# Kernel tuning notes

Hardware: AMD Instinct MI355X
Metric: run time of the kernel (lower is better)

Reference implementation:

```python
import jax, jax.numpy as jnp
import numpy as np

# Dimensions (match init_kwargs / input_specs)
B, T, H, S, R, E = 4, 2048, 1024, 512, 16, 4
F = 6 + 2 * R           # engine_state_feature_dim
ETA = 0.1               # impression_rate
ACC_DECAY = 0.99        # accumulator EMA decay
EPS = 1e-6


def setup_inputs() -> dict:
    key = jax.random.key(0)
    ks = jax.random.split(key, 20)
    n = jax.random.normal
    x = n(ks[0], (B, T, H), jnp.float32)
    # ComplexLinear signal_proj: hidden -> state
    sig_Wr = n(ks[1], (H, S), jnp.float32) / np.sqrt(H).astype(np.float32)
    sig_Wi = n(ks[2], (H, S), jnp.float32) / np.sqrt(H).astype(np.float32)
    sig_br = jnp.zeros((S,), jnp.float32)
    sig_bi = jnp.zeros((S,), jnp.float32)
    # Per-engine complex state projection [E, S, R] and diagonal complex decay [E, R]
    A_r = n(ks[3], (E, S, R), jnp.float32) / np.sqrt(S).astype(np.float32)
    A_i = n(ks[4], (E, S, R), jnp.float32) / np.sqrt(S).astype(np.float32)
    mag = 0.90 + 0.09 * jax.random.uniform(ks[5], (E, R), jnp.float32)
    ph = (2.0 * np.pi) * jax.random.uniform(ks[6], (E, R), jnp.float32)
    lam_r = mag * jnp.cos(ph)
    lam_i = mag * jnp.sin(ph)
    # Per-engine ComplexLinear: feature(F) -> hidden(H)
    eh_Wr = n(ks[7], (E, F, H), jnp.float32) / np.sqrt(F).astype(np.float32)
    eh_Wi = n(ks[8], (E, F, H), jnp.float32) / np.sqrt(F).astype(np.float32)
    eh_br = jnp.zeros((E, H), jnp.float32)
    eh_bi = jnp.zeros((E, H), jnp.float32)
    # Engine fusion ComplexLinear: E*H -> H
    fu_Wr = n(ks[9], (E * H, H), jnp.float32) / np.sqrt(E * H).astype(np.float32)
    fu_Wi = n(ks[10], (E * H, H), jnp.float32) / np.sqrt(E * H).astype(np.float32)
    fu_br = jnp.zeros((H,), jnp.float32)
    fu_bi = jnp.zeros((H,), jnp.float32)
    # Gate: Linear(4H -> H)
    g_W = n(ks[11], (4 * H, H), jnp.float32) / np.sqrt(4 * H).astype(np.float32)
    g_b = jnp.zeros((H,), jnp.float32)
    return dict(x=x, sig_Wr=sig_Wr, sig_Wi=sig_Wi, sig_br=sig_br, sig_bi=sig_bi,
                A_r=A_r, A_i=A_i, lam_r=lam_r, lam_i=lam_i,
                eh_Wr=eh_Wr, eh_Wi=eh_Wi, eh_br=eh_br, eh_bi=eh_bi,
                fu_Wr=fu_Wr, fu_Wi=fu_Wi, fu_br=fu_br, fu_bi=fu_bi,
                g_W=g_W, g_b=g_b)


def _run_engines(ur, ui, lam_r, lam_i):
    """Complex diagonal recurrence over time for all engines jointly.
    ur, ui: [E,B,T,R] complex drive. Returns per-step features [E,B,T,F] (real, imag)."""
    lr = lam_r[:, None, :]  # [E,1,R]
    li = lam_i[:, None, :]

    def step(carry, u):
        hr, hi, acc = carry                      # [E,B,R], [E,B,R], [E,B]
        ur_t, ui_t = u                           # [E,B,R]
        nhr = (1.0 - ETA) * (lr * hr - li * hi) + ETA * ur_t
        nhi = (1.0 - ETA) * (lr * hi + li * hr) + ETA * ui_t
        mag2 = nhr * nhr + nhi * nhi             # [E,B,R]
        m_mean = jnp.mean(mag2, axis=-1)         # [E,B]
        nacc = ACC_DECAY * acc + (1.0 - ACC_DECAY) * m_mean
        inv = jax.lax.rsqrt(m_mean + EPS)[..., None]
        hnr, hni = nhr * inv, nhi * inv          # rms-normalized complex state
        z = jnp.zeros_like(m_mean)
        scal_r = jnp.stack([hnr.mean(-1), hni.mean(-1),
                            jnp.sqrt(m_mean + EPS),
                            jnp.sqrt(jnp.max(mag2, axis=-1) + EPS),
                            nacc, jnp.log1p(nacc)], axis=-1)   # [E,B,6]
        scal_i = jnp.stack([hni.mean(-1), -hnr.mean(-1), z, z, z, z], axis=-1)
        fr = jnp.concatenate([scal_r, hnr, hni], axis=-1)      # [E,B,F]
        fi = jnp.concatenate([scal_i, hni, -hnr], axis=-1)
        return (nhr, nhi, nacc), (fr, fi)

    init = (jnp.zeros((E, B, R), ur.dtype), jnp.zeros((E, B, R), ur.dtype),
            jnp.zeros((E, B), ur.dtype))
    u_seq = (jnp.moveaxis(ur, 2, 0), jnp.moveaxis(ui, 2, 0))   # [T,E,B,R]
    _, (frs, fis) = jax.lax.scan(step, init, u_seq)
    return jnp.moveaxis(frs, 0, 2), jnp.moveaxis(fis, 0, 2)    # [E,B,T,F]


def reference(x, sig_Wr, sig_Wi, sig_br, sig_bi, A_r, A_i, lam_r, lam_i,
              eh_Wr, eh_Wi, eh_br, eh_bi, fu_Wr, fu_Wi, fu_br, fu_bi, g_W, g_b):
    # Complex signal projection of real input: z = (Wr + i Wi)^T x + b
    zr = x @ sig_Wr + sig_br                     # [B,T,S]
    zi = x @ sig_Wi + sig_bi
    # Complex per-engine drive u = A^H-style complex matmul: [E,B,T,R]
    ur = jnp.einsum('bts,esr->ebtr', zr, A_r) - jnp.einsum('bts,esr->ebtr', zi, A_i)
    ui = jnp.einsum('bts,esr->ebtr', zr, A_i) + jnp.einsum('bts,esr->ebtr', zi, A_r)
    fr, fi = _run_engines(ur, ui, lam_r, lam_i)  # [E,B,T,F]
    # Per-engine ComplexLinear feature -> hidden
    yr = (jnp.einsum('ebtf,efh->ebth', fr, eh_Wr)
          - jnp.einsum('ebtf,efh->ebth', fi, eh_Wi)) + eh_br[:, None, None, :]
    yi = (jnp.einsum('ebtf,efh->ebth', fr, eh_Wi)
          + jnp.einsum('ebtf,efh->ebth', fi, eh_Wr)) + eh_bi[:, None, None, :]
    # Concat engines along feature axis -> [B,T,E*H]
    yr_c = jnp.moveaxis(yr, 0, 2).reshape(B, T, E * H)
    yi_c = jnp.moveaxis(yi, 0, 2).reshape(B, T, E * H)
    # Engine fusion ComplexLinear
    frf = yr_c @ fu_Wr - yi_c @ fu_Wi + fu_br    # [B,T,H]
    fif = yr_c @ fu_Wi + yi_c @ fu_Wr + fu_bi
    mag = jnp.sqrt(frf * frf + fif * fif + EPS)
    g = jax.nn.sigmoid(jnp.concatenate([x, frf, fif, mag], axis=-1) @ g_W + g_b)
    return g * frf + (1.0 - g) * x
```

## Files before the change

### kernel.cpp

```cpp
#include <hip/hip_runtime.h>
#include <stdint.h>

#define B_ 4
#define T_ 2048
#define H_ 1024
#define S_ 512
#define R_ 16
#define E_ 4
#define F_ 38
#define BT_ (B_*T_)
#define KF_ 320

typedef __attribute__((ext_vector_type(8))) __bf16 bf16x8;
typedef __attribute__((ext_vector_type(4))) float f32x4;

static __device__ __forceinline__ unsigned short f2bf(float f) {
    unsigned int u = __float_as_uint(f);
    unsigned int r = (u + 0x7fffu + ((u >> 16) & 1u)) >> 16;
    return (unsigned short)r;
}

static __device__ __forceinline__ void gload_lds16(const unsigned short* g, unsigned short* l) {
    __builtin_amdgcn_global_load_lds(
        (const __attribute__((address_space(1))) unsigned int*)g,
        (__attribute__((address_space(3))) unsigned int*)l, 16, 0, 0);
}

template<int EPI>
__global__ __launch_bounds__(256) void k_gemm(
    const unsigned short* __restrict__ A, int lda,
    const unsigned short* __restrict__ BT, int ldb,
    float* __restrict__ C, int ldc,
    const float* __restrict__ bias, int K,
    size_t sA, size_t sB, size_t sC, int nbx,
    const float* __restrict__ aux1, const float* __restrict__ aux2,
    unsigned short* __restrict__ auxO)
{
    A  += (size_t)blockIdx.z * sA;
    BT += (size_t)blockIdx.z * sB;
    C  += (size_t)blockIdx.z * sC;

    int bx, by;
    {
        const int f = blockIdx.x;
        const int nwg = gridDim.x;
        int s;
        if ((nwg & 7) == 0) {
            const int q = nwg >> 3;
            s = (f & 7) * q + (f >> 3);
        } else s = f;
        by = s / nbx; bx = s - by * nbx;
    }

    __shared__ unsigned short As[2 * 4096];
    __shared__ unsigned short Bs[2 * 4096];
    const int tid = threadIdx.x;
    const int l = tid & 63;
    const int wv = tid >> 6;
    const int wm = wv >> 1, wn = wv & 1;
    const int m16 = l & 15, kg = l >> 4;
    const size_t bm = (size_t)by * 128;
    const size_t bn = (size_t)bx * 128;

    const int slab0 = wv * 2, slab1 = wv * 2 + 1;
    const int rIn = l >> 2;
    const int kOff = (l & 3) * 8;
    const unsigned short* gA0 = A + (bm + slab0 * 16 + rIn) * (size_t)lda + kOff;
    const unsigned short* gA1 = A + (bm + slab1 * 16 + rIn) * (size_t)lda + kOff;
    const unsigned short* gB0 = BT + (bn + slab0 * 16 + rIn) * (size_t)ldb + kOff;
    const unsigned short* gB1 = BT + (bn + slab1 * 16 + rIn) * (size_t)ldb + kOff;
    const int sOffA0 = slab0 * 512, sOffA1 = slab1 * 512;

    f32x4 acc[4][4];
#pragma unroll
    for (int i = 0; i < 4; ++i)
#pragma unroll
        for (int j = 0; j < 4; ++j) acc[i][j] = (f32x4){0.f, 0.f, 0.f, 0.f};

    const int nkt = K >> 5;
    gload_lds16(gA0, As + sOffA0);
    gload_lds16(gA1, As + sOffA1);
    gload_lds16(gB0, Bs + sOffA0);
    gload_lds16(gB1, Bs + sOffA1);
    gA0 += 32; gA1 += 32; gB0 += 32; gB1 += 32;
    __syncthreads();

    for (int kt = 0; kt < nkt; ++kt) {
        const int cur = (kt & 1) * 4096;
        const int nxt = 4096 - cur;
        if (kt + 1 < nkt) {
            gload_lds16(gA0, As + nxt + sOffA0);
            gload_lds16(gA1, As + nxt + sOffA1);
            gload_lds16(gB0, Bs + nxt + sOffA0);
            gload_lds16(gB1, Bs + nxt + sOffA1);
            gA0 += 32; gA1 += 32; gB0 += 32; gB1 += 32;
        }
        bf16x8 af[4], bfr[4];
#pragma unroll
        for (int i = 0; i < 4; ++i)
            af[i] = *(const bf16x8*)&As[cur + (wm * 64 + i * 16 + m16) * 32 + kg * 8];
#pragma unroll
        for (int j = 0; j < 4; ++j)
            bfr[j] = *(const bf16x8*)&Bs[cur + (wn * 64 + j * 16 + m16) * 32 + kg * 8];
#pragma unroll
        for (int i = 0; i < 4; ++i)
#pragma unroll
            for (int j = 0; j < 4; ++j)
                acc[i][j] = __builtin_amdgcn_mfma_f32_16x16x32_bf16(af[i], bfr[j], acc[i][j], 0, 0, 0);
        __syncthreads();
    }

#pragma unroll
    for (int j = 0; j < 4; ++j) {
        const size_t col = bn + wn * 64 + j * 16 + m16;
        const float bv = (EPI == 1) ? 0.f : (bias ? bias[col] : 0.f);
#pragma unroll
        for (int i = 0; i < 4; ++i) {
            const size_t row0 = bm + wm * 64 + i * 16 + kg * 4;
#pragma unroll
            for (int p = 0; p < 4; ++p) {
                const size_t row = row0 + p;
                if constexpr (EPI == 0) {
                    C[row * (size_t)ldc + col] = acc[i][j][p] + bv;
                } else if constexpr (EPI == 1) {
                    atomicAdd(&C[row * (size_t)ldc + col], acc[i][j][p]);
                } else if constexpr (EPI == 2) {
                    const float v = acc[i][j][p] + bv;
                    const float w = __shfl_xor(v, 1, 64);
                    const int h = (int)(col >> 1);
                    if ((col & 1) == 0) {
                        C[row * 1024 + h] = v;
                        auxO[row * 4096 + 1024 + h] = f2bf(v);
                    } else {
                        auxO[row * 4096 + 2048 + h] = f2bf(v);
                        auxO[row * 4096 + 3072 + h] = f2bf(sqrtf(w * w + v * v + 1e-6f));
                    }
                } else {
                    const float z = acc[i][j][p] + bv;
                    const float g = 1.f / (1.f + __expf(-z));
                    const float fr = aux1[row * 1024 + col];
                    const float xv = aux2[row * 1024 + col];
                    C[row * 1024 + col] = fmaf(g, fr - xv, xv);
                }
            }
        }
    }
}

__global__ __launch_bounds__(256) void k_cast_x(const float* __restrict__ x,
                                                unsigned short* __restrict__ Abig)
{
    const int gid = blockIdx.x * 256 + threadIdx.x;
    const int row = gid >> 8;
    const int c4 = (gid & 255) << 2;
    float4 v = *(const float4*)&x[(size_t)row * H_ + c4];
    ushort4 o;
    o.x = f2bf(v.x); o.y = f2bf(v.y); o.z = f2bf(v.z); o.w = f2bf(v.w);
    *(ushort4*)&Abig[(size_t)row * 4096 + c4] = o;
}

__global__ __launch_bounds__(256) void k_gwt(const float* __restrict__ gW,
                                             unsigned short* __restrict__ gWT)
{
    __shared__ float tile[32][33];
    const int tx = threadIdx.x & 31, ty = threadIdx.x >> 5;
    const int k0 = blockIdx.x * 32, n0 = blockIdx.y * 32;
#pragma unroll
    for (int q = 0; q < 4; ++q) {
        int kk = ty * 4 + q;
        tile[kk][tx] = gW[(size_t)(k0 + kk) * H_ + n0 + tx];
    }
    __syncthreads();
#pragma unroll
    for (int q = 0; q < 4; ++q) {
        int nn = ty * 4 + q;
        gWT[(size_t)(n0 + nn) * 4096 + k0 + tx] = f2bf(tile[tx][nn]);
    }
}

__global__ __launch_bounds__(64) void k_wu(const float* __restrict__ sigWr,
                                           const float* __restrict__ sigWi,
                                           const float* __restrict__ A_r,
                                           const float* __restrict__ A_i,
                                           unsigned short* __restrict__ WuT)
{
    __shared__ float swr[S_], swi[S_];
    const int h = blockIdx.x;
    const int tid = threadIdx.x;
    for (int s = tid; s < S_; s += 64) {
        swr[s] = sigWr[(size_t)h * S_ + s];
        swi[s] = sigWi[(size_t)h * S_ + s];
    }
    __syncthreads();
    const int e = tid >> 4, r = tid & 15;
    float a0 = 0.f, a1 = 0.f;
    for (int s = 0; s < S_; ++s) {
        float ar = A_r[((size_t)(e * S_ + s)) * R_ + r];
        float ai = A_i[((size_t)(e * S_ + s)) * R_ + r];
        float wr = swr[s], wi = swi[s];
        a0 += wr * ar - wi * ai;
        a1 += wr * ai + wi * ar;
    }
    WuT[(size_t)tid * H_ + h] = f2bf(a0);
    WuT[(size_t)(64 + tid) * H_ + h] = f2bf(a1);
}

__global__ __launch_bounds__(64) void k_bu(const float* __restrict__ sigbr,
                                           const float* __restrict__ sigbi,
                                           const float* __restrict__ A_r,
                                           const float* __restrict__ A_i,
                                           float* __restrict__ b_u)
{
    const int n = blockIdx.x;
    const int lane = threadIdx.x;
    const int m = n & 63;
    const int e = m >> 4, r = m & 15;
    const bool hi = n >= 64;
    float acc = 0.f;
    for (int s = lane; s < S_; s += 64) {
        float ar = A_r[((size_t)(e * S_ + s)) * R_ + r];
        float ai = A_i[((size_t)(e * S_ + s)) * R_ + r];
        float br = sigbr[s], bi = sigbi[s];
        acc += hi ? (br * ai + bi * ar) : (br * ar - bi * ai);
    }
#pragma unroll
    for (int st = 32; st; st >>= 1) acc += __shfl_down(acc, st, 64);
    if (lane == 0) b_u[n] = acc;
}

__global__ __launch_bounds__(256) void k_uinit(const float* __restrict__ b_u,
                                               float* __restrict__ U)
{
    const int gid = blockIdx.x * 256 + threadIdx.x;
    U[gid] = b_u[gid & 127];
}

__global__ __launch_bounds__(256) void k_prepA(const float* __restrict__ ehWr,
                                               const float* __restrict__ ehWi,
                                               const float* __restrict__ ehbr,
                                               const float* __restrict__ ehbi,
                                               unsigned short* __restrict__ Ac)
{
    const int gid = blockIdx.x * 256 + threadIdx.x;
    const int e = gid >> 16;
    const int rem = gid & 65535;
    const int row = rem >> 9;
    const int k = (rem & 511) << 2;
    float4 f = {0.f, 0.f, 0.f, 0.f};
    if (row < F_) {
        const float* src = (k < 1024) ? ehWr + ((size_t)(e * F_ + row)) * 1024 + k
                                      : ehWi + ((size_t)(e * F_ + row)) * 1024 + (k - 1024);
        f = *(const float4*)src;
    } else if (row == F_) {
        const float* src = (k < 1024) ? ehbr + (size_t)e * 1024 + k
                                      : ehbi + (size_t)e * 1024 + (k - 1024);
        f = *(const float4*)src;
    }
    ushort4 o;
    o.x = f2bf(f.x); o.y = f2bf(f.y); o.z = f2bf(f.z); o.w = f2bf(f.w);
    *(ushort4*)&Ac[(size_t)gid * 4] = o;
}

__global__ __launch_bounds__(256) void k_prepB(const float* __restrict__ fuWr,
                                               const float* __restrict__ fuWi,
                                               unsigned short* __restrict__ Bc)
{
    __shared__ float tR[32][33], tI[32][33];
    const int e = blockIdx.z;
    const int k0 = blockIdx.x * 32;
    const int h0 = blockIdx.y * 32;
    const int tx = threadIdx.x & 31, ty = threadIdx.x >> 5;
    const float* fr = fuWr + ((size_t)e * 1024 + k0) * 1024 + h0;
    const float* fi = fuWi + ((size_t)e * 1024 + k0) * 1024 + h0;
#pragma unroll
    for (int q = 0; q < 4; ++q) {
        int kk = ty * 4 + q;
        tR[kk][tx] = fr[(size_t)kk * 1024 + tx];
        tI[kk][tx] = fi[(size_t)kk * 1024 + tx];
    }
    __syncthreads();
    unsigned short* Be = Bc + (size_t)e * 2048 * 2048;
#pragma unroll
    for (int q = 0; q < 4; ++q) {
        int rr = ty * 4 + q;
        float vR = tR[tx][rr], vI = tI[tx][rr];
        size_t rowLo = (size_t)(h0 + rr) * 2048;
        size_t rowHi = (size_t)(1024 + h0 + rr) * 2048;
        Be[rowLo + k0 + tx]        = f2bf(vR);
        Be[rowLo + 1024 + k0 + tx] = f2bf(-vI);
        Be[rowHi + k0 + tx]        = f2bf(vI);
        Be[rowHi + 1024 + k0 + tx] = f2bf(vR);
    }
}

__global__ __launch_bounds__(256) void k_w2t(const float* __restrict__ C,
                                             unsigned short* __restrict__ W2T)
{
    const int gid = blockIdx.x * 256 + threadIdx.x;
    const int n = gid / KF_;
    const int k = gid - n * KF_;
    const int h = n >> 1;
    const int s = n & 1;
    float v = 0.f;
    if (k < 304) {
        const int fp = (k < 152) ? k : k - 152;
        const int e = fp / F_;
        const int f = fp - e * F_;
        const float* Ce = C + ((size_t)e * 128 + f) * 2048;
        const float mr = Ce[h], mi = Ce[1024 + h];
        if (s == 0) v = (k < 152) ? mr : -mi;
        else        v = (k < 152) ? mi :  mr;
    }
    W2T[gid] = f2bf(v);
}

__global__ __launch_bounds__(256) void k_b2(const float* __restrict__ fubr,
                                            const float* __restrict__ fubi,
                                            const float* __restrict__ C,
                                            float* __restrict__ b2)
{
    const int n = blockIdx.x * 256 + threadIdx.x;
    const int h = n >> 1;
    const int s = n & 1;
    const int colOld = s * 1024 + h;
    float v = s ? fubi[h] : fubr[h];
#pragma unroll
    for (int e = 0; e < 4; ++e)
        v += C[(size_t)e * 128 * 2048 + (size_t)F_ * 2048 + colOld];
    b2[n] = v;
}

__global__ __launch_bounds__(64) void k_scan(const float* __restrict__ U,
                                             const float* __restrict__ lam_r,
                                             const float* __restrict__ lam_i,
                                             float* __restrict__ Hr, float* __restrict__ Hi)
{
    const int wid = blockIdx.x;
    const int b = wid >> 6, ch = wid & 63;
    const int lane = threadIdx.x;
    const float cr = 0.9f * lam_r[ch];
    const float ci = 0.9f * lam_i[ch];
    const float* Ub = U + (size_t)b * T_ * 128;
    const int t0 = lane * 32;
    float ur[32], ui[32];
#pragma unroll
    for (int j = 0; j < 32; ++j) {
        ur[j] = Ub[(size_t)(t0 + j) * 128 + ch];
        ui[j] = Ub[(size_t)(t0 + j) * 128 + 64 + ch];
    }
    float hr = 0.f, hi = 0.f;
#pragma unroll
    for (int j = 0; j < 32; ++j) {
        float nr = fmaf(cr, hr, fmaf(-ci, hi, 0.1f * ur[j]));
        float ni = fmaf(cr, hi, fmaf(ci, hr, 0.1f * ui[j]));
        hr = nr; hi = ni;
    }
    float dr = cr, di = ci;
#pragma unroll
    for (int q = 0; q < 5; ++q) { float t = dr*dr - di*di; di = 2.f*dr*di; dr = t; }
    float xr = hr, xi = hi;
#pragma unroll
    for (int st = 1; st < 64; st <<= 1) {
        float yr = __shfl_up(xr, (unsigned)st, 64);
        float yi = __shfl_up(xi, (unsigned)st, 64);
        if (lane >= st) {
            float nxr = fmaf(dr, yr, fmaf(-di, yi, xr));
            float nxi = fmaf(dr, yi, fmaf(di, yr, xi));
            xr = nxr; xi = nxi;
        }
        float t = dr*dr - di*di; di = 2.f*dr*di; dr = t;
    }
    float ir = __shfl_up(xr, 1u, 64);
    float ii = __shfl_up(xi, 1u, 64);
    if (lane == 0) { ir = 0.f; ii = 0.f; }
    hr = ir; hi = ii;
    float* HrB = Hr + (size_t)b * T_ * 64;
    float* HiB = Hi + (size_t)b * T_ * 64;
#pragma unroll
    for (int j = 0; j < 32; ++j) {
        float nr = fmaf(cr, hr, fmaf(-ci, hi, 0.1f * ur[j]));
        float ni = fmaf(cr, hi, fmaf(ci, hr, 0.1f * ui[j]));
        HrB[(size_t)(t0 + j) * 64 + ch] = nr;
        HiB[(size_t)(t0 + j) * 64 + ch] = ni;
        hr = nr; hi = ni;
    }
}

__global__ __launch_bounds__(256) void k_feat(const float* __restrict__ Hr,
                                              const float* __restrict__ Hi,
                                              unsigned short* __restrict__ Fcat,
                                              float* __restrict__ Mbuf)
{
    const int gid = blockIdx.x * 256 + threadIdx.x;
    const int e = gid & 3;
    const int bt = gid >> 2;
    const float* hr = Hr + (size_t)bt * 64 + e * 16;
    const float* hi = Hi + (size_t)bt * 64 + e * 16;
    float nr[16], ni[16];
#pragma unroll
    for (int q = 0; q < 4; ++q) {
        float4 vr = ((const float4*)hr)[q];
        float4 vi = ((const float4*)hi)[q];
        nr[q*4+0]=vr.x; nr[q*4+1]=vr.y; nr[q*4+2]=vr.z; nr[q*4+3]=vr.w;
        ni[q*4+0]=vi.x; ni[q*4+1]=vi.y; ni[q*4+2]=vi.z; ni[q*4+3]=vi.w;
    }
    float sum = 0.f, mx = 0.f, sr = 0.f, si = 0.f;
#pragma unroll
    for (int i = 0; i < 16; ++i) {
        float m2 = nr[i] * nr[i] + ni[i] * ni[i];
        sum += m2; mx = fmaxf(mx, m2);
        sr += nr[i]; si += ni[i];
    }
    const float mm = sum * 0.0625f;
    const float inv = rsqrtf(mm + 1e-6f);
    const int b = bt >> 11, t = bt & (T_ - 1);
    Mbuf[(size_t)(e * 4 + b) * T_ + t] = mm;
    unsigned short* Fp = Fcat + (size_t)bt * KF_;
    const int br = e * F_, bi2 = 152 + e * F_;
    const float mhr = sr * 0.0625f * inv;
    const float mhi = si * 0.0625f * inv;
    Fp[br + 0] = f2bf(mhr);
    Fp[br + 1] = f2bf(mhi);
    Fp[br + 2] = f2bf(sqrtf(mm + 1e-6f));
    Fp[br + 3] = f2bf(sqrtf(mx + 1e-6f));
    Fp[bi2 + 0] = f2bf(mhi);
    Fp[bi2 + 1] = f2bf(-mhr);
#pragma unroll
    for (int i = 0; i < 16; ++i) {
        float a = nr[i] * inv, c = ni[i] * inv;
        Fp[br + 6 + i]   = f2bf(a);
        Fp[br + 22 + i]  = f2bf(c);
        Fp[bi2 + 6 + i]  = f2bf(c);
        Fp[bi2 + 22 + i] = f2bf(-a);
    }
}

__global__ __launch_bounds__(256) void k_acc(const float* __restrict__ Mbuf,
                                             unsigned short* __restrict__ Fcat)
{
    const int w = blockIdx.x * 4 + (threadIdx.x >> 6);
    const int lane = threadIdx.x & 63;
    const int e = w >> 2, b = w & 3;
    const float* mp = Mbuf + (size_t)(e * 4 + b) * T_ + lane * 32;
    float m[32];
#pragma unroll
    for (int j = 0; j < 32; ++j) m[j] = mp[j];
    float s = 0.f;
#pragma unroll
    for (int j = 0; j < 32; ++j) s = fmaf(0.99f, s, 0.01f * m[j]);
    float d = 0.99f;
#pragma unroll
    for (int q = 0; q < 5; ++q) d = d * d;
    float x = s;
#pragma unroll
    for (int st = 1; st < 64; st <<= 1) {
        float y = __shfl_up(x, (unsigned)st, 64);
        if (lane >= st) x = fmaf(d, y, x);
        d = d * d;
    }
    float init = __shfl_up(x, 1u, 64);
    if (lane == 0) init = 0.f;
    float acc = init;
#pragma unroll
    for (int j = 0; j < 32; ++j) {
        acc = fmaf(0.99f, acc, 0.01f * m[j]);
        const int t = lane * 32 + j;
        size_t ro = ((size_t)(b * T_ + t)) * KF_ + e * F_;
        Fcat[ro + 4] = f2bf(acc);
        Fcat[ro + 5] = f2bf(log1pf(acc));
    }
}

extern "C" void kernel_launch(void* const* d_in, const int* in_sizes, int n_in,
                              void* d_out, int out_size, void* d_ws, size_t ws_size,
                              hipStream_t stream)
{
    const float* x     = (const float*)d_in[0];
    const float* sigWr = (const float*)d_in[1];
    const float* sigWi = (const float*)d_in[2];
    const float* sigbr = (const float*)d_in[3];
    const float* sigbi = (const float*)d_in[4];
    const float* A_r   = (const float*)d_in[5];
    const float* A_i   = (const float*)d_in[6];
    const float* lam_r = (const float*)d_in[7];
    const float* lam_i = (const float*)d_in[8];
    const float* ehWr  = (const float*)d_in[9];
    const float* ehWi  = (const float*)d_in[10];
    const float* ehbr  = (const float*)d_in[11];
    const float* ehbi  = (const float*)d_in[12];
    const float* fuWr  = (const float*)d_in[13];
    const float* fuWi  = (const float*)d_in[14];
    const float* fubr  = (const float*)d_in[15];
    const float* fubi  = (const float*)d_in[16];
    const float* gW    = (const float*)d_in[17];
    const float* gb    = (const float*)d_in[18];

    char* ws = (char*)d_ws;
    size_t off = 0;
    auto alloc = [&](size_t bytes) -> void* {
        void* p = ws + off;
        off = (off + bytes + 255) & ~(size_t)255;
        return p;
    };
    unsigned short* Abig = (unsigned short*)alloc((size_t)BT_ * 4096 * 2);
    float* FRFr          = (float*)alloc((size_t)BT_ * 1024 * 4);
    unsigned short* Fcat = (unsigned short*)alloc((size_t)BT_ * KF_ * 2);
    float* U             = (float*)alloc((size_t)BT_ * 128 * 4);
    float* Hr            = (float*)alloc((size_t)BT_ * 64 * 4);
    float* Hi            = (float*)alloc((size_t)BT_ * 64 * 4);
    float* Mbuf          = (float*)alloc((size_t)16 * T_ * 4);
    unsigned short* WuT  = (unsigned short*)alloc((size_t)128 * H_ * 2);
    float* b_u           = (float*)alloc(128 * 4);
    unsigned short* W2T  = (unsigned short*)alloc((size_t)2048 * KF_ * 2);
    float* b2            = (float*)alloc(2048 * 4);
    unsigned short* gWT  = (unsigned short*)alloc((size_t)H_ * 4096 * 2);
    unsigned short* Acomp= (unsigned short*)alloc((size_t)4 * 128 * 2048 * 2);
    unsigned short* Bcomp= (unsigned short*)alloc((size_t)4 * 2048 * 2048 * 2);
    float* Ccomp         = (float*)alloc((size_t)4 * 128 * 2048 * 4);
    if (off > ws_size) return;

    hipMemsetAsync(Fcat, 0, (size_t)BT_ * KF_ * 2, stream);

    k_cast_x<<<dim3(BT_ * H_ / 4 / 256), dim3(256), 0, stream>>>(x, Abig);
    k_gwt<<<dim3(128, 32), dim3(256), 0, stream>>>(gW, gWT);
    k_wu<<<dim3(H_), dim3(64), 0, stream>>>(sigWr, sigWi, A_r, A_i, WuT);
    k_bu<<<dim3(128), dim3(64), 0, stream>>>(sigbr, sigbi, A_r, A_i, b_u);
    k_prepA<<<dim3(1024), dim3(256), 0, stream>>>(ehWr, ehWi, ehbr, ehbi, Acomp);
    k_prepB<<<dim3(32, 32, 4), dim3(256), 0, stream>>>(fuWr, fuWi, Bcomp);

    k_gemm<0><<<dim3(16, 1, 4), dim3(256), 0, stream>>>(
        Acomp, 2048, Bcomp, 2048, Ccomp, 2048, (const float*)nullptr, 2048,
        (size_t)128 * 2048, (size_t)2048 * 2048, (size_t)128 * 2048, 16,
        nullptr, nullptr, nullptr);

    k_w2t<<<dim3(2048 * KF_ / 256), dim3(256), 0, stream>>>(Ccomp, W2T);
    k_b2<<<dim3(8), dim3(256), 0, stream>>>(fubr, fubi, Ccomp, b2);

    k_uinit<<<dim3(BT_ * 128 / 256), dim3(256), 0, stream>>>(b_u, U);
    k_gemm<1><<<dim3(64, 1, 4), dim3(256), 0, stream>>>(
        Abig, 4096, WuT, H_, U, 128, (const float*)nullptr, 256,
        (size_t)256, (size_t)256, (size_t)0, 1, nullptr, nullptr, nullptr);

    k_scan<<<dim3(B_ * 64), dim3(64), 0, stream>>>(U, lam_r, lam_i, Hr, Hi);
    k_feat<<<dim3(BT_ * E_ / 256), dim3(256), 0, stream>>>(Hr, Hi, Fcat, Mbuf);
    k_acc<<<dim3(4), dim3(256), 0, stream>>>(Mbuf, Fcat);

    k_gemm<2><<<dim3(1024, 1, 1), dim3(256), 0, stream>>>(
        Fcat, KF_, W2T, KF_, FRFr, 1024, b2, KF_,
        (size_t)0, (size_t)0, (size_t)0, 16, nullptr, nullptr, Abig);

    k_gemm<3><<<dim3(512, 1, 1), dim3(256), 0, stream>>>(
        Abig, 4096, gWT, 4096, (float*)d_out, 1024, gb, 4096,
        (size_t)0, (size_t)0, (size_t)0, 8, FRFr, x, nullptr);
}
```

Baseline: 392.0 us.

## Deepen GEMM LDS pipeline, split-K the fusion precompute, transpose U layout

The GEMM kernel gains a templated pipeline depth. Up to four LDS stages are kept in flight, with explicit vmcnt waits and raw barriers replacing the per-iteration __syncthreads. The weight-composition GEMM is split along K into four chunks accumulated with atomics into a zeroed buffer, which raises its block count from 64 to 256. The U projection now writes a transposed layout so the scan can read time-contiguous float4 vectors instead of strided scalars. These changes add LDS usage, which can lower occupancy, plus atomic traffic and an extra memset.

```diff
diff --git a/kernel.cpp b/kernel.cpp
--- a/kernel.cpp
+++ b/kernel.cpp
@@ -26,19 +26,20 @@
         (__attribute__((address_space(3))) unsigned int*)l, 16, 0, 0);
 }
 
-template<int EPI>
+template<int EPI, int DEPTH>
 __global__ __launch_bounds__(256) void k_gemm(
     const unsigned short* __restrict__ A, int lda,
     const unsigned short* __restrict__ BT, int ldb,
     float* __restrict__ C, int ldc,
     const float* __restrict__ bias, int K,
-    size_t sA, size_t sB, size_t sC, int nbx,
+    size_t sA, size_t sB, size_t sC, size_t sA2, size_t sB2, int nbx,
     const float* __restrict__ aux1, const float* __restrict__ aux2,
     unsigned short* __restrict__ auxO)
 {
-    A  += (size_t)blockIdx.z * sA;
-    BT += (size_t)blockIdx.z * sB;
-    C  += (size_t)blockIdx.z * sC;
+    const int z1 = blockIdx.z >> 2, z0 = blockIdx.z & 3;
+    A  += (size_t)z1 * sA + (size_t)z0 * sA2;
+    BT += (size_t)z1 * sB + (size_t)z0 * sB2;
+    C  += (size_t)z1 * sC;
 
     int bx, by;
     {
@@ -52,8 +53,8 @@
         by = s / nbx; bx = s - by * nbx;
     }
 
-    __shared__ unsigned short As[2 * 4096];
-    __shared__ unsigned short Bs[2 * 4096];
+    __shared__ unsigned short As[DEPTH * 4096];
+    __shared__ unsigned short Bs[DEPTH * 4096];
     const int tid = threadIdx.x;
     const int l = tid & 63;
     const int wv = tid >> 6;
@@ -78,23 +79,37 @@
         for (int j = 0; j < 4; ++j) acc[i][j] = (f32x4){0.f, 0.f, 0.f, 0.f};
 
     const int nkt = K >> 5;
-    gload_lds16(gA0, As + sOffA0);
-    gload_lds16(gA1, As + sOffA1);
-    gload_lds16(gB0, Bs + sOffA0);
-    gload_lds16(gB1, Bs + sOffA1);
-    gA0 += 32; gA1 += 32; gB0 += 32; gB1 += 32;
-    __syncthreads();
-
-    for (int kt = 0; kt < nkt; ++kt) {
-        const int cur = (kt & 1) * 4096;
-        const int nxt = 4096 - cur;
-        if (kt + 1 < nkt) {
-            gload_lds16(gA0, As + nxt + sOffA0);
-            gload_lds16(gA1, As + nxt + sOffA1);
-            gload_lds16(gB0, Bs + nxt + sOffA0);
-            gload_lds16(gB1, Bs + nxt + sOffA1);
+#pragma unroll
+    for (int p = 0; p < DEPTH - 1; ++p) {
+        if (p < nkt) {
+            const int o = p * 4096;
+            gload_lds16(gA0, As + o + sOffA0);
+            gload_lds16(gA1, As + o + sOffA1);
+            gload_lds16(gB0, Bs + o + sOffA0);
+            gload_lds16(gB1, Bs + o + sOffA1);
             gA0 += 32; gA1 += 32; gB0 += 32; gB1 += 32;
         }
+    }
+
+    for (int kt = 0; kt < nkt; ++kt) {
+        __builtin_amdgcn_s_barrier();
+        if (kt + DEPTH - 1 < nkt) {
+            const int o = ((kt + DEPTH - 1) % DEPTH) * 4096;
+            gload_lds16(gA0, As + o + sOffA0);
+            gload_lds16(gA1, As + o + sOffA1);
+            gload_lds16(gB0, Bs + o + sOffA0);
+            gload_lds16(gB1, Bs + o + sOffA1);
+            gA0 += 32; gA1 += 32; gB0 += 32; gB1 += 32;
+        }
+        const int rem = nkt - 1 - kt;
+        const int ahead = rem < (DEPTH - 1) ? rem : (DEPTH - 1);
+        if (ahead >= 3)      asm volatile("s_waitcnt vmcnt(12)" ::: "memory");
+        else if (ahead == 2) asm volatile("s_waitcnt vmcnt(8)" ::: "memory");
+        else if (ahead == 1) asm volatile("s_waitcnt vmcnt(4)" ::: "memory");
+        else                 asm volatile("s_waitcnt vmcnt(0)" ::: "memory");
+        __builtin_amdgcn_s_barrier();
+
+        const int cur = (kt % DEPTH) * 4096;
         bf16x8 af[4], bfr[4];
 #pragma unroll
         for (int i = 0; i < 4; ++i)
@@ -107,13 +122,12 @@
 #pragma unroll
             for (int j = 0; j < 4; ++j)
                 acc[i][j] = __builtin_amdgcn_mfma_f32_16x16x32_bf16(af[i], bfr[j], acc[i][j], 0, 0, 0);
-        __syncthreads();
     }
 
 #pragma unroll
     for (int j = 0; j < 4; ++j) {
         const size_t col = bn + wn * 64 + j * 16 + m16;
-        const float bv = (EPI == 1) ? 0.f : (bias ? bias[col] : 0.f);
+        const float bv = (EPI == 1 || EPI == 4) ? 0.f : (bias ? bias[col] : 0.f);
 #pragma unroll
         for (int i = 0; i < 4; ++i) {
             const size_t row0 = bm + wm * 64 + i * 16 + kg * 4;
@@ -124,6 +138,8 @@
                     C[row * (size_t)ldc + col] = acc[i][j][p] + bv;
                 } else if constexpr (EPI == 1) {
                     atomicAdd(&C[row * (size_t)ldc + col], acc[i][j][p]);
+                } else if constexpr (EPI == 4) {
+                    atomicAdd(&C[col * (size_t)ldc + row], acc[i][j][p]);
                 } else if constexpr (EPI == 2) {
                     const float v = acc[i][j][p] + bv;
                     const float w = __shfl_xor(v, 1, 64);
@@ -232,7 +248,7 @@
                                                float* __restrict__ U)
 {
     const int gid = blockIdx.x * 256 + threadIdx.x;
-    U[gid] = b_u[gid & 127];
+    U[gid] = b_u[gid >> 13];
 }
 
 __global__ __launch_bounds__(256) void k_prepA(const float* __restrict__ ehWr,
@@ -340,13 +356,16 @@
     const int lane = threadIdx.x;
     const float cr = 0.9f * lam_r[ch];
     const float ci = 0.9f * lam_i[ch];
-    const float* Ub = U + (size_t)b * T_ * 128;
+    const float* Ur = U + (size_t)ch * BT_ + (size_t)b * T_;
+    const float* Uc = U + (size_t)(64 + ch) * BT_ + (size_t)b * T_;
     const int t0 = lane * 32;
     float ur[32], ui[32];
 #pragma unroll
-    for (int j = 0; j < 32; ++j) {
-        ur[j] = Ub[(size_t)(t0 + j) * 128 + ch];
-        ui[j] = Ub[(size_t)(t0 + j) * 128 + 64 + ch];
+    for (int q = 0; q < 8; ++q) {
+        float4 vr = *(const float4*)&Ur[t0 + q * 4];
+        float4 vi = *(const float4*)&Uc[t0 + q * 4];
+        ur[q*4+0]=vr.x; ur[q*4+1]=vr.y; ur[q*4+2]=vr.z; ur[q*4+3]=vr.w;
+        ui[q*4+0]=vi.x; ui[q*4+1]=vi.y; ui[q*4+2]=vi.z; ui[q*4+3]=vi.w;
     }
     float hr = 0.f, hi = 0.f;
 #pragma unroll
@@ -520,6 +539,7 @@
     if (off > ws_size) return;
 
     hipMemsetAsync(Fcat, 0, (size_t)BT_ * KF_ * 2, stream);
+    hipMemsetAsync(Ccomp, 0, (size_t)4 * 128 * 2048 * 4, stream);
 
     k_cast_x<<<dim3(BT_ * H_ / 4 / 256), dim3(256), 0, stream>>>(x, Abig);
     k_gwt<<<dim3(128, 32), dim3(256), 0, stream>>>(gW, gWT);
@@ -528,28 +548,31 @@
     k_prepA<<<dim3(1024), dim3(256), 0, stream>>>(ehWr, ehWi, ehbr, ehbi, Acomp);
     k_prepB<<<dim3(32, 32, 4), dim3(256), 0, stream>>>(fuWr, fuWi, Bcomp);
 
-    k_gemm<0><<<dim3(16, 1, 4), dim3(256), 0, stream>>>(
-        Acomp, 2048, Bcomp, 2048, Ccomp, 2048, (const float*)nullptr, 2048,
-        (size_t)128 * 2048, (size_t)2048 * 2048, (size_t)128 * 2048, 16,
-        nullptr, nullptr, nullptr);
+    k_gemm<1, 4><<<dim3(16, 1, 16), dim3(256), 0, stream>>>(
+        Acomp, 2048, Bcomp, 2048, Ccomp, 2048, (const float*)nullptr, 512,
+        (size_t)128 * 2048, (size_t)2048 * 2048, (size_t)128 * 2048,
+        (size_t)512, (size_t)512, 16, nullptr, nullptr, nullptr);
 
     k_w2t<<<dim3(2048 * KF_ / 256), dim3(256), 0, stream>>>(Ccomp, W2T);
     k_b2<<<dim3(8), dim3(256), 0, stream>>>(fubr, fubi, Ccomp, b2);
 
     k_uinit<<<dim3(BT_ * 128 / 256), dim3(256), 0, stream>>>(b_u, U);
-    k_gemm<1><<<dim3(64, 1, 4), dim3(256), 0, stream>>>(
-        Abig, 4096, WuT, H_, U, 128, (const float*)nullptr, 256,
-        (size_t)256, (size_t)256, (size_t)0, 1, nullptr, nullptr, nullptr);
+    k_gemm<4, 4><<<dim3(64, 1, 4), dim3(256), 0, stream>>>(
+        Abig, 4096, WuT, H_, U, BT_, (const float*)nullptr, 256,
+        (size_t)0, (size_t)0, (size_t)0, (size_t)256, (size_t)256, 1,
+        nullptr, nullptr, nullptr);
 
     k_scan<<<dim3(B_ * 64), dim3(64), 0, stream>>>(U, lam_r, lam_i, Hr, Hi);
     k_feat<<<dim3(BT_ * E_ / 256), dim3(256), 0, stream>>>(Hr, Hi, Fcat, Mbuf);
     k_acc<<<dim3(4), dim3(256), 0, stream>>>(Mbuf, Fcat);
 
-    k_gemm<2><<<dim3(1024, 1, 1), dim3(256), 0, stream>>>(
+    k_gemm<2, 2><<<dim3(1024, 1, 1), dim3(256), 0, stream>>>(
         Fcat, KF_, W2T, KF_, FRFr, 1024, b2, KF_,
-        (size_t)0, (size_t)0, (size_t)0, 16, nullptr, nullptr, Abig);
-
-    k_gemm<3><<<dim3(512, 1, 1), dim3(256), 0, stream>>>(
+        (size_t)0, (size_t)0, (size_t)0, (size_t)0, (size_t)0, 16,
+        nullptr, nullptr, Abig);
+
+    k_gemm<3, 4><<<dim3(512, 1, 1), dim3(256), 0, stream>>>(
         Abig, 4096, gWT, 4096, (float*)d_out, 1024, gb, 4096,
-        (size_t)0, (size_t)0, (size_t)0, 8, FRFr, x, nullptr);
-}
+        (size_t)0, (size_t)0, (size_t)0, (size_t)0, (size_t)0, 8,
+        FRFr, x, nullptr);
+}
```

After: 418.1 us. +6.7%, slower.
